# Kernel optimization log

Measured on AMD Instinct MI355X. Metric: run time of the kernel, lower is better.

The kernel has to match this reference:

```python
import jax, jax.numpy as jnp
import numpy as np

N = 20000
E = 320000
F_IN = 256
HID = 32
HEADS = 8
EDGE_DIM = HID // 4  # 8
NEG_SLOPE = 0.2


def _gat_conv(x, src, dst, e_emb, W, att_s, att_d, W_e, att_e, bias, H, C):
    """PyG-style GATConv with edge_dim, add_self_loops=True (fill_value='mean'), concat heads."""
    n = x.shape[0]
    loop = jnp.arange(n, dtype=src.dtype)
    # self-loop edge_attr = scatter-mean of edge_attr by dst (0 for isolated nodes)
    deg = jax.ops.segment_sum(jnp.ones_like(dst, dtype=x.dtype), dst, num_segments=n)
    e_mean = jax.ops.segment_sum(e_emb, dst, num_segments=n) / jnp.maximum(deg, 1.0)[:, None]
    src_a = jnp.concatenate([src, loop])
    dst_a = jnp.concatenate([dst, loop])
    e_all = jnp.concatenate([e_emb, e_mean], axis=0)  # [E+N, edge_dim]

    h = (x @ W).reshape(n, H, C)                      # [N,H,C]
    a_src = jnp.einsum('nhc,hc->nh', h, att_s)        # [N,H]
    a_dst = jnp.einsum('nhc,hc->nh', h, att_d)
    he = (e_all @ W_e).reshape(-1, H, C)              # [E+N,H,C]
    a_edge = jnp.einsum('ehc,hc->eh', he, att_e)      # [E+N,H]

    alpha = jax.nn.leaky_relu(a_src[src_a] + a_dst[dst_a] + a_edge, NEG_SLOPE)
    # segment softmax over destination nodes
    amax = jax.ops.segment_max(alpha, dst_a, num_segments=n)
    alpha = jnp.exp(alpha - amax[dst_a])
    denom = jax.ops.segment_sum(alpha, dst_a, num_segments=n)
    alpha = alpha / (denom[dst_a] + 1e-16)

    msg = h[src_a] * alpha[:, :, None]                # [E+N,H,C]
    out = jax.ops.segment_sum(msg, dst_a, num_segments=n)  # [N,H,C]
    return out.reshape(n, H * C) + bias


def setup_inputs() -> dict:
    key = jax.random.key(0)
    ks = jax.random.split(key, 16)

    def glorot(k, shape):
        fan_in, fan_out = shape[0], shape[-1]
        s = np.sqrt(6.0 / (fan_in + fan_out))
        return jax.random.uniform(k, shape, jnp.float32, -s, s)

    x = jax.random.normal(ks[0], (N, F_IN), jnp.float32)
    edge_index = jax.random.randint(ks[1], (2, E), 0, N, jnp.int32)
    edge_attr = jax.random.uniform(ks[2], (E, 2), jnp.float32)

    # spatial_embed: Linear(2 -> EDGE_DIM)
    Wse = glorot(ks[3], (2, EDGE_DIM))
    bse = jnp.zeros((EDGE_DIM,), jnp.float32)
    # conv1: in=F_IN, heads=HEADS, out=HID, edge_dim=EDGE_DIM
    W1 = glorot(ks[4], (F_IN, HEADS * HID))
    as1 = glorot(ks[5], (HEADS, HID))
    ad1 = glorot(ks[6], (HEADS, HID))
    We1 = glorot(ks[7], (EDGE_DIM, HEADS * HID))
    ae1 = glorot(ks[8], (HEADS, HID))
    b1 = jnp.zeros((HEADS * HID,), jnp.float32)
    # conv2: in=HEADS*HID, heads=1, out=HID
    W2 = glorot(ks[9], (HEADS * HID, HID))
    as2 = glorot(ks[10], (1, HID))
    ad2 = glorot(ks[11], (1, HID))
    We2 = glorot(ks[12], (EDGE_DIM, HID))
    ae2 = glorot(ks[13], (1, HID))
    b2 = jnp.zeros((HID,), jnp.float32)

    return {"x": x, "edge_index": edge_index, "edge_attr": edge_attr,
            "Wse": Wse, "bse": bse,
            "W1": W1, "as1": as1, "ad1": ad1, "We1": We1, "ae1": ae1, "b1": b1,
            "W2": W2, "as2": as2, "ad2": ad2, "We2": We2, "ae2": ae2, "b2": b2}


def reference(x, edge_index, edge_attr, Wse, bse,
              W1, as1, ad1, We1, ae1, b1,
              W2, as2, ad2, We2, ae2, b2):
    src, dst = edge_index[0], edge_index[1]
    e = jax.nn.relu(edge_attr @ Wse + bse)            # [E, EDGE_DIM]
    h = _gat_conv(x, src, dst, e, W1, as1, ad1, We1, ae1, b1, HEADS, HID)
    h = jax.nn.relu(h)                                # dropout inactive (eval)
    out = _gat_conv(h, src, dst, e, W2, as2, ad2, We2, ae2, b2, 1, HID)
    return out
```

## Files before the change

### kernel.cpp

```cpp
#include <hip/hip_runtime.h>
#include <hip/hip_bf16.h>
#include <hip/hip_fp16.h>
#include <float.h>


typedef short v8s __attribute__((ext_vector_type(8)));
typedef float v4f __attribute__((ext_vector_type(4)));

__device__ __forceinline__ ushort f2bf(float f) {
  unsigned u = __float_as_uint(f);
  u = (u + 0x7FFF + ((u >> 16) & 1)) >> 16;
  return (ushort)u;
}
__device__ __forceinline__ float bf2f(ushort h) {
  return __uint_as_float(((unsigned)h) << 16);
}
__device__ __forceinline__ unsigned pk2bf(float lo, float hi) {
  return (unsigned)f2bf(lo) | ((unsigned)f2bf(hi) << 16);
}
__device__ __forceinline__ unsigned pk2h(float lo, float hi) {
  return (unsigned)__half_as_ushort(__float2half(lo)) |
         ((unsigned)__half_as_ushort(__float2half(hi)) << 16);
}

__global__ __launch_bounds__(256) void k_pre(const int* __restrict__ dst,
                                             const float* __restrict__ W1,
                                             const float* __restrict__ We1,
                                             const float* __restrict__ ae1,
                                             const float* __restrict__ We2,
                                             const float* __restrict__ ae2,
                                             int* __restrict__ deg,
                                             ushort* __restrict__ Bt,
                                             float* __restrict__ M1,
                                             float* __restrict__ m2,
                                             int E, int DB) {
  int b = blockIdx.x;
  if (b < DB) {
    int e = b * 256 + threadIdx.x;
    if (e < E) atomicAdd(&deg[dst[e]], 1);
    return;
  }
  if (b == DB + 64) {
    int t = threadIdx.x;
    if (t < 64) {
      int k = t >> 3, h = t & 7;
      float s = 0.f;
      for (int c = 0; c < 32; c++) s += We1[k * 256 + h * 32 + c] * ae1[h * 32 + c];
      M1[k * 8 + h] = s;
    } else if (t < 72) {
      int k = t - 64;
      float s = 0.f;
      for (int c = 0; c < 32; c++) s += We2[k * 32 + c] * ae2[c];
      m2[k] = s;
    }
    return;
  }
  int b2 = b - DB;
  __shared__ float tile[32][33];
  int bx = b2 & 7, by = b2 >> 3;
  int tx = threadIdx.x & 31, ty = threadIdx.x >> 5;
  for (int r = ty; r < 32; r += 8)
    tile[r][tx] = W1[(size_t)(by * 32 + r) * 256 + bx * 32 + tx];
  __syncthreads();
  for (int r = ty; r < 32; r += 8)
    Bt[(size_t)(bx * 32 + r) * 256 + by * 32 + tx] = f2bf(tile[tx][r]);
}

__global__ __launch_bounds__(1024) void k_scan(const int* __restrict__ deg,
                                               int* __restrict__ row_ptr,
                                               int* __restrict__ cursor, int N) {
  __shared__ int part[1024];
  int tid = threadIdx.x;
  int chunk = (N + 1023) / 1024;
  int lo = tid * chunk;
  if (lo > N) lo = N;
  int hi = lo + chunk;
  if (hi > N) hi = N;
  int s = 0;
  for (int i = lo; i < hi; i++) { s += deg[i]; cursor[i] = 0; }
  part[tid] = s;
  __syncthreads();
  for (int off = 1; off < 1024; off <<= 1) {
    int v = 0;
    if (tid >= off) v = part[tid - off];
    __syncthreads();
    part[tid] += v;
    __syncthreads();
  }
  int base = part[tid] - s;
  for (int i = lo; i < hi; i++) { row_ptr[i] = base; base += deg[i]; }
  if (tid == 1023) row_ptr[N] = part[1023];
}

__global__ void k_scatter(const int* __restrict__ src, const int* __restrict__ dst,
                          const float* __restrict__ ea,
                          const float* __restrict__ Wse, const float* __restrict__ bse,
                          const float* __restrict__ M1, const float* __restrict__ m2,
                          const int* __restrict__ row_ptr, int* __restrict__ cursor,
                          char* __restrict__ rec, int E) {
  __shared__ float sW[16], sb[8], sM[64], sm2[8];
  int t = threadIdx.x;
  if (t < 16) sW[t] = Wse[t];
  if (t < 8) sb[t] = bse[t];
  if (t < 64) sM[t] = M1[t];
  if (t >= 64 && t < 72) sm2[t - 64] = m2[t - 64];
  __syncthreads();
  int i = blockIdx.x * blockDim.x + t;
  if (i >= E) return;
  float2 av = ((const float2*)ea)[i];
  float e8[8];
#pragma unroll
  for (int k = 0; k < 8; k++)
    e8[k] = fmaxf(av.x * sW[k] + av.y * sW[8 + k] + sb[k], 0.f);
  float o[8];
#pragma unroll
  for (int h = 0; h < 8; h++) {
    float s = 0.f;
#pragma unroll
    for (int k = 0; k < 8; k++) s += e8[k] * sM[k * 8 + h];
    o[h] = s;
  }
  float s2 = 0.f;
#pragma unroll
  for (int k = 0; k < 8; k++) s2 += e8[k] * sm2[k];
  int d = dst[i];
  int pos = row_ptr[d] + atomicAdd(&cursor[d], 1);
  uint4 w0, w1;
  w0.x = (unsigned)src[i];
  w0.y = pk2h(o[0], o[1]);
  w0.z = pk2h(o[2], o[3]);
  w0.w = pk2h(o[4], o[5]);
  w1.x = pk2h(o[6], o[7]);
  w1.y = __float_as_uint(s2);
  w1.z = 0; w1.w = 0;
  *(uint4*)(rec + (size_t)pos * 32)      = w0;
  *(uint4*)(rec + (size_t)pos * 32 + 16) = w1;
}

__global__ __launch_bounds__(256) void k_gemm1_mfma(const float* __restrict__ A,
                                                    const ushort* __restrict__ Bt,
                                                    const float* __restrict__ as1,
                                                    const float* __restrict__ ad1,
                                                    ushort* __restrict__ h1b,
                                                    float* __restrict__ asv,
                                                    float* __restrict__ adv, int M) {
  __shared__ ushort sA[64 * 40];
  __shared__ ushort sB[256 * 40];
  __shared__ float sas[256], sad[256];
  int t = threadIdx.x;
  int wave = t >> 6, lane = t & 63;
  int m0 = blockIdx.x * 64;
  int c = lane & 15, kg = lane >> 4;
  sas[t] = as1[t];
  sad[t] = ad1[t];
  v4f acc[4][4];
#pragma unroll
  for (int a = 0; a < 4; a++)
#pragma unroll
    for (int b = 0; b < 4; b++) acc[a][b] = (v4f)(0.f);
  int arow = t >> 2;
  int akoff = (t & 3) * 8;
  bool aval = (m0 + arow) < M;
  const float* aptr = A + (size_t)(m0 + arow) * 256 + akoff;
  const ushort* bptr = Bt + (size_t)t * 256;
  for (int k0 = 0; k0 < 256; k0 += 32) {
    float4 v0 = make_float4(0.f, 0.f, 0.f, 0.f), v1 = v0;
    if (aval) { v0 = *(const float4*)(aptr + k0); v1 = *(const float4*)(aptr + k0 + 4); }
    unsigned* dst32 = (unsigned*)&sA[arow * 40 + akoff];
    dst32[0] = pk2bf(v0.x, v0.y);
    dst32[1] = pk2bf(v0.z, v0.w);
    dst32[2] = pk2bf(v1.x, v1.y);
    dst32[3] = pk2bf(v1.z, v1.w);
    *(v8s*)&sB[t * 40 + 0]  = *(const v8s*)(bptr + k0 + 0);
    *(v8s*)&sB[t * 40 + 8]  = *(const v8s*)(bptr + k0 + 8);
    *(v8s*)&sB[t * 40 + 16] = *(const v8s*)(bptr + k0 + 16);
    *(v8s*)&sB[t * 40 + 24] = *(const v8s*)(bptr + k0 + 24);
    __syncthreads();
    v8s af[4], bfr[4];
#pragma unroll
    for (int mt = 0; mt < 4; mt++) af[mt] = *(v8s*)&sA[(mt * 16 + c) * 40 + kg * 8];
#pragma unroll
    for (int nt = 0; nt < 4; nt++) bfr[nt] = *(v8s*)&sB[(wave * 64 + nt * 16 + c) * 40 + kg * 8];
#pragma unroll
    for (int mt = 0; mt < 4; mt++)
#pragma unroll
      for (int nt = 0; nt < 4; nt++)
        acc[mt][nt] = __builtin_amdgcn_mfma_f32_16x16x32_bf16(af[mt], bfr[nt], acc[mt][nt], 0, 0, 0);
    __syncthreads();
  }
  int colbase = wave * 64;
#pragma unroll
  for (int mt = 0; mt < 4; mt++) {
#pragma unroll
    for (int i = 0; i < 4; i++) {
      int m = m0 + mt * 16 + kg * 4 + i;
      if (m < M) {
#pragma unroll
        for (int nt = 0; nt < 4; nt++)
          h1b[(size_t)m * 256 + colbase + nt * 16 + c] = f2bf(acc[mt][nt][i]);
      }
      float s1a = acc[mt][0][i] * sas[colbase + c]      + acc[mt][1][i] * sas[colbase + 16 + c];
      float s2a = acc[mt][0][i] * sad[colbase + c]      + acc[mt][1][i] * sad[colbase + 16 + c];
      float s1b = acc[mt][2][i] * sas[colbase + 32 + c] + acc[mt][3][i] * sas[colbase + 48 + c];
      float s2b = acc[mt][2][i] * sad[colbase + 32 + c] + acc[mt][3][i] * sad[colbase + 48 + c];
#pragma unroll
      for (int o = 1; o < 16; o <<= 1) {
        s1a += __shfl_xor(s1a, o);
        s2a += __shfl_xor(s2a, o);
        s1b += __shfl_xor(s1b, o);
        s2b += __shfl_xor(s2b, o);
      }
      if (c == 0 && m < M) {
        asv[(size_t)m * 8 + 2 * wave]     = s1a;
        adv[(size_t)m * 8 + 2 * wave]     = s2a;
        asv[(size_t)m * 8 + 2 * wave + 1] = s1b;
        adv[(size_t)m * 8 + 2 * wave + 1] = s2b;
      }
    }
  }
}

__global__ __launch_bounds__(64) void k_conv1(
    const int* __restrict__ row_ptr, const char* __restrict__ rec,
    const float* __restrict__ asv, const float* __restrict__ adv,
    const ushort* __restrict__ h1b, const float* __restrict__ b1,
    ushort* __restrict__ h2b, int N) {
  int n = blockIdx.x;
  int lane = threadIdx.x;
  int h = lane >> 3;
  int sub = lane & 7;
  int hh = lane & 7;
  __shared__ float sw[64 * 8];
  __shared__ int ssrc[64];
  __shared__ float sm[8], sl[8], sadv[8], smean[8];
  int begin = row_ptr[n], end = row_ptr[n + 1];
  int degr = end - begin;
  if (lane < 8) { sm[lane] = -FLT_MAX; sl[lane] = 0.f; sadv[lane] = adv[(size_t)n * 8 + lane]; }
  float aedsum = 0.f;
  float4 acc = make_float4(0.f, 0.f, 0.f, 0.f);
  for (int cs = begin; cs < end; cs += 64) {
    int c = min(64, end - cs);
    __syncthreads();
    if (lane < c) ssrc[lane] = *(const int*)(rec + (size_t)(cs + lane) * 32);
    __syncthreads();
    for (int idx = lane; idx < c * 8; idx += 64) {
      int el = idx >> 3;
      float ae = __half2float(*(const __half*)(rec + (size_t)(cs + el) * 32 + 4 + hh * 2));
      aedsum += ae;
      float a = asv[(size_t)ssrc[el] * 8 + hh] + sadv[hh] + ae;
      a = a > 0.f ? a : 0.2f * a;
      sw[idx] = a;
    }
    __syncthreads();
    float mloc = -FLT_MAX;
    for (int el = sub; el < c; el += 8) mloc = fmaxf(mloc, sw[el * 8 + h]);
#pragma unroll
    for (int o = 1; o < 8; o <<= 1) mloc = fmaxf(mloc, __shfl_xor(mloc, o));
    float mold = sm[h];
    float mnew = fmaxf(mold, mloc);
    float scale = __expf(mold - mnew);
    float lloc = 0.f;
    for (int el = sub; el < c; el += 8) {
      float w = __expf(sw[el * 8 + h] - mnew);
      sw[el * 8 + h] = w;
      lloc += w;
    }
#pragma unroll
    for (int o = 1; o < 8; o <<= 1) lloc += __shfl_xor(lloc, o);
    __syncthreads();
    if (sub == 0) { sm[h] = mnew; sl[h] = sl[h] * scale + lloc; }
    acc.x *= scale; acc.y *= scale; acc.z *= scale; acc.w *= scale;
#pragma unroll 2
    for (int el = 0; el < c; el++) {
      float w = sw[el * 8 + h];
      ushort4 hv = *(const ushort4*)(h1b + (size_t)ssrc[el] * 256 + lane * 4);
      acc.x += w * bf2f(hv.x);
      acc.y += w * bf2f(hv.y);
      acc.z += w * bf2f(hv.z);
      acc.w += w * bf2f(hv.w);
    }
  }
  aedsum += __shfl_xor(aedsum, 8);
  aedsum += __shfl_xor(aedsum, 16);
  aedsum += __shfl_xor(aedsum, 32);
  float invd = 1.f / (float)(degr > 1 ? degr : 1);
  if (lane < 8) smean[lane] = aedsum * invd;
  __syncthreads();
  float a_self = asv[(size_t)n * 8 + h] + sadv[h] + smean[h];
  a_self = a_self > 0.f ? a_self : 0.2f * a_self;
  float mold = sm[h];
  float mnew = fmaxf(mold, a_self);
  float scale = __expf(mold - mnew);
  float w_self = __expf(a_self - mnew);
  float l_fin = sl[h] * scale + w_self;
  ushort4 hs = *(const ushort4*)(h1b + (size_t)n * 256 + lane * 4);
  acc.x = acc.x * scale + w_self * bf2f(hs.x);
  acc.y = acc.y * scale + w_self * bf2f(hs.y);
  acc.z = acc.z * scale + w_self * bf2f(hs.z);
  acc.w = acc.w * scale + w_self * bf2f(hs.w);
  float inv = 1.f / (l_fin + 1e-16f);
  float4 bv = *(const float4*)(b1 + lane * 4);
  ushort4 o4;
  o4.x = f2bf(fmaxf(acc.x * inv + bv.x, 0.f));
  o4.y = f2bf(fmaxf(acc.y * inv + bv.y, 0.f));
  o4.z = f2bf(fmaxf(acc.z * inv + bv.z, 0.f));
  o4.w = f2bf(fmaxf(acc.w * inv + bv.w, 0.f));
  *(ushort4*)(h2b + (size_t)n * 256 + lane * 4) = o4;
}

__global__ __launch_bounds__(256) void k_gemm2(const ushort* __restrict__ h2b,
                                               const float* __restrict__ W2,
                                               const float* __restrict__ as2,
                                               const float* __restrict__ ad2,
                                               float* __restrict__ g2,
                                               float* __restrict__ asv2,
                                               float* __restrict__ adv2, int N) {
  __shared__ float xs[8 * 256];
  __shared__ float sas[32], sad[32];
  int t = threadIdx.x;
  if (t < 32) { sas[t] = as2[t]; sad[t] = ad2[t]; }
  int n0 = blockIdx.x * 8;
  for (int idx = t; idx < 8 * 256; idx += 256) {
    int node = n0 + (idx >> 8);
    xs[idx] = (node < N) ? bf2f(h2b[(size_t)node * 256 + (idx & 255)]) : 0.f;
  }
  __syncthreads();
  int j = t >> 5, cc = t & 31;
  int node = n0 + j;
  float acc = 0.f;
#pragma unroll 8
  for (int k = 0; k < 256; k++) acc += xs[j * 256 + k] * W2[k * 32 + cc];
  float s1 = acc * sas[cc], s2 = acc * sad[cc];
#pragma unroll
  for (int o = 1; o < 32; o <<= 1) {
    s1 += __shfl_xor(s1, o);
    s2 += __shfl_xor(s2, o);
  }
  if (node < N) {
    g2[(size_t)node * 32 + cc] = acc;
    if (cc == 0) { asv2[node] = s1; adv2[node] = s2; }
  }
}

__global__ __launch_bounds__(64) void k_conv2(
    const int* __restrict__ row_ptr, const char* __restrict__ rec,
    const float* __restrict__ asv2, const float* __restrict__ adv2,
    const float* __restrict__ g2, const float* __restrict__ b2,
    float* __restrict__ out, int N) {
  int n = blockIdx.x;
  int lane = threadIdx.x;
  int sub = lane >> 3, q = lane & 7;
  __shared__ float sw[64];
  __shared__ int ssrc[64];
  int begin = row_ptr[n], end = row_ptr[n + 1];
  int degr = end - begin;
  float advn = adv2[n];
  float m = -FLT_MAX, l = 0.f, aedsum = 0.f;
  float4 acc = make_float4(0.f, 0.f, 0.f, 0.f);
  for (int cs = begin; cs < end; cs += 64) {
    int c = min(64, end - cs);
    __syncthreads();
    float a = -FLT_MAX;
    if (lane < c) {
      const char* rp = rec + (size_t)(cs + lane) * 32;
      int s = *(const int*)rp;
      ssrc[lane] = s;
      float ae = *(const float*)(rp + 20);
      aedsum += ae;
      a = asv2[s] + advn + ae;
      a = a > 0.f ? a : 0.2f * a;
    }
    float cm = a;
#pragma unroll
    for (int o = 1; o < 64; o <<= 1) cm = fmaxf(cm, __shfl_xor(cm, o));
    float nm = fmaxf(m, cm);
    float sc = __expf(m - nm);
    float w = (lane < c) ? __expf(a - nm) : 0.f;
    float cl = w;
#pragma unroll
    for (int o = 1; o < 64; o <<= 1) cl += __shfl_xor(cl, o);
    l = l * sc + cl;
    m = nm;
    sw[lane] = w;
    __syncthreads();
    acc.x *= sc; acc.y *= sc; acc.z *= sc; acc.w *= sc;
    for (int el = sub; el < c; el += 8) {
      float w2 = sw[el];
      const float4 gv = *(const float4*)(g2 + (size_t)ssrc[el] * 32 + q * 4);
      acc.x += w2 * gv.x; acc.y += w2 * gv.y; acc.z += w2 * gv.z; acc.w += w2 * gv.w;
    }
  }
#pragma unroll
  for (int o = 1; o < 64; o <<= 1) aedsum += __shfl_xor(aedsum, o);
  float invd = 1.f / (float)(degr > 1 ? degr : 1);
  float a_self = asv2[n] + advn + aedsum * invd;
  a_self = a_self > 0.f ? a_self : 0.2f * a_self;
  float nm = fmaxf(m, a_self);
  float sc = __expf(m - nm);
  float w_self = __expf(a_self - nm);
  l = l * sc + w_self;
  acc.x *= sc; acc.y *= sc; acc.z *= sc; acc.w *= sc;
  if (sub == 0) {
    const float4 gv = *(const float4*)(g2 + (size_t)n * 32 + q * 4);
    acc.x += w_self * gv.x; acc.y += w_self * gv.y;
    acc.z += w_self * gv.z; acc.w += w_self * gv.w;
  }
#pragma unroll
  for (int o = 8; o < 64; o <<= 1) {
    acc.x += __shfl_xor(acc.x, o);
    acc.y += __shfl_xor(acc.y, o);
    acc.z += __shfl_xor(acc.z, o);
    acc.w += __shfl_xor(acc.w, o);
  }
  if (lane < 8) {
    float inv = 1.f / (l + 1e-16f);
    float4 bv = *(const float4*)(b2 + lane * 4);
    float4 o4;
    o4.x = acc.x * inv + bv.x;
    o4.y = acc.y * inv + bv.y;
    o4.z = acc.z * inv + bv.z;
    o4.w = acc.w * inv + bv.w;
    *(float4*)(out + (size_t)n * 32 + lane * 4) = o4;
  }
}

extern "C" void kernel_launch(void* const* d_in, const int* in_sizes, int n_in,
                              void* d_out, int out_size, void* d_ws, size_t ws_size,
                              hipStream_t stream) {
  (void)n_in; (void)out_size; (void)ws_size;
  const float* x   = (const float*)d_in[0];
  const int*   ei  = (const int*)d_in[1];
  const float* ea  = (const float*)d_in[2];
  const float* Wse = (const float*)d_in[3];
  const float* bse = (const float*)d_in[4];
  const float* W1  = (const float*)d_in[5];
  const float* as1 = (const float*)d_in[6];
  const float* ad1 = (const float*)d_in[7];
  const float* We1 = (const float*)d_in[8];
  const float* ae1 = (const float*)d_in[9];
  const float* b1  = (const float*)d_in[10];
  const float* W2  = (const float*)d_in[11];
  const float* as2 = (const float*)d_in[12];
  const float* ad2 = (const float*)d_in[13];
  const float* We2 = (const float*)d_in[14];
  const float* ae2 = (const float*)d_in[15];
  const float* b2  = (const float*)d_in[16];
  const int N = in_sizes[0] / 256;
  const int E = in_sizes[1] / 2;
  const int* src = ei;
  const int* dst = ei + E;

  char* base = (char*)d_ws;
  size_t off = 0;
  auto alloc = [&](size_t bytes) -> char* {
    off = (off + 255) & ~(size_t)255;
    char* p = base + off;
    off += bytes;
    return p;
  };
  int*   deg      = (int*)alloc((size_t)N * 4);
  int*   cursor   = (int*)alloc((size_t)N * 4);
  int* row_ptr    = (int*)alloc((size_t)(N + 1) * 4);
  char* rec       = alloc((size_t)E * 32);
  ushort* W1T     = (ushort*)alloc((size_t)256 * 256 * 2);
  ushort* h1b     = (ushort*)alloc((size_t)N * 256 * 2);
  float* asv1     = (float*)alloc((size_t)N * 8 * 4);
  float* adv1     = (float*)alloc((size_t)N * 8 * 4);
  ushort* h2b     = (ushort*)alloc((size_t)N * 256 * 2);
  float* g2       = (float*)alloc((size_t)N * 32 * 4);
  float* asv2     = (float*)alloc((size_t)N * 4);
  float* adv2     = (float*)alloc((size_t)N * 4);
  float* M1       = (float*)alloc(64 * 4);
  float* m2       = (float*)alloc(8 * 4);

  const int DB = (E + 255) / 256;
  hipMemsetAsync(deg, 0, (size_t)N * 4, stream);
  k_pre<<<DB + 65, 256, 0, stream>>>(dst, W1, We1, ae1, We2, ae2, deg, W1T, M1, m2, E, DB);
  k_scan<<<1, 1024, 0, stream>>>(deg, row_ptr, cursor, N);
  k_scatter<<<DB, 256, 0, stream>>>(src, dst, ea, Wse, bse, M1, m2, row_ptr, cursor,
                                    rec, E);
  k_gemm1_mfma<<<(N + 63) / 64, 256, 0, stream>>>(x, W1T, as1, ad1, h1b, asv1, adv1, N);
  k_conv1<<<N, 64, 0, stream>>>(row_ptr, rec, asv1, adv1, h1b, b1, h2b, N);
  k_gemm2<<<(N + 7) / 8, 256, 0, stream>>>(h2b, W2, as2, ad2, g2, asv2, adv2, N);
  k_conv2<<<N, 64, 0, stream>>>(row_ptr, rec, asv2, adv2, g2, b2, (float*)d_out, N);
}
```

Before: 256.2 us.

## Merge edge scatter with GEMM1 launch and fuse GEMM2 into conv1 epilogue

The edge-record scatter and the layer-1 MFMA GEMM now run as two roles of one combined launch selected by block index, so the independent work overlaps and one launch is removed. The layer-2 projection (256->32 matmul plus attention dot products) moves into the conv1 epilogue: each node's hidden vector stays in shared memory and is multiplied by a pre-blocked copy of W2 built in k_pre. This drops the bf16 h2b round trip through global memory and the separate gemm2 kernel. The cost is that every conv1 block re-reads all of W2 (32 KB, likely cache-resident) with one 64-lane block per node, and the mega kernel's shared-memory footprint is sized for the GEMM role.

```diff
diff --git a/kernel.cpp b/kernel.cpp
--- a/kernel.cpp
+++ b/kernel.cpp
@@ -29,10 +29,12 @@
                                              const float* __restrict__ ae1,
                                              const float* __restrict__ We2,
                                              const float* __restrict__ ae2,
+                                             const float* __restrict__ W2,
                                              int* __restrict__ deg,
                                              ushort* __restrict__ Bt,
                                              float* __restrict__ M1,
                                              float* __restrict__ m2,
+                                             float* __restrict__ W2B,
                                              int E, int DB) {
   int b = blockIdx.x;
   if (b < DB) {
@@ -42,6 +44,10 @@
   }
   if (b == DB + 64) {
     int t = threadIdx.x;
+    for (int i = t; i < 8192; i += 256) {
+      int k = i >> 5, cc = i & 31;
+      W2B[(size_t)(k >> 2) * 128 + cc * 4 + (k & 3)] = W2[(size_t)k * 32 + cc];
+    }
     if (t < 64) {
       int k = t >> 3, h = t & 7;
       float s = 0.f;
@@ -92,62 +98,63 @@
   if (tid == 1023) row_ptr[N] = part[1023];
 }
 
-__global__ void k_scatter(const int* __restrict__ src, const int* __restrict__ dst,
-                          const float* __restrict__ ea,
-                          const float* __restrict__ Wse, const float* __restrict__ bse,
-                          const float* __restrict__ M1, const float* __restrict__ m2,
-                          const int* __restrict__ row_ptr, int* __restrict__ cursor,
-                          char* __restrict__ rec, int E) {
-  __shared__ float sW[16], sb[8], sM[64], sm2[8];
+__global__ __launch_bounds__(256) void k_mega1(
+    const float* __restrict__ A, const ushort* __restrict__ Bt,
+    const float* __restrict__ as1, const float* __restrict__ ad1,
+    ushort* __restrict__ h1b, float* __restrict__ asv, float* __restrict__ adv, int M,
+    const int* __restrict__ src, const int* __restrict__ dst,
+    const float* __restrict__ ea, const float* __restrict__ Wse,
+    const float* __restrict__ bse, const float* __restrict__ M1,
+    const float* __restrict__ m2, const int* __restrict__ row_ptr,
+    int* __restrict__ cursor, char* __restrict__ rec, int E, int GB) {
+  __shared__ __align__(16) char smem[27648];
   int t = threadIdx.x;
-  if (t < 16) sW[t] = Wse[t];
-  if (t < 8) sb[t] = bse[t];
-  if (t < 64) sM[t] = M1[t];
-  if (t >= 64 && t < 72) sm2[t - 64] = m2[t - 64];
-  __syncthreads();
-  int i = blockIdx.x * blockDim.x + t;
-  if (i >= E) return;
-  float2 av = ((const float2*)ea)[i];
-  float e8[8];
-#pragma unroll
-  for (int k = 0; k < 8; k++)
-    e8[k] = fmaxf(av.x * sW[k] + av.y * sW[8 + k] + sb[k], 0.f);
-  float o[8];
-#pragma unroll
-  for (int h = 0; h < 8; h++) {
-    float s = 0.f;
-#pragma unroll
-    for (int k = 0; k < 8; k++) s += e8[k] * sM[k * 8 + h];
-    o[h] = s;
-  }
-  float s2 = 0.f;
-#pragma unroll
-  for (int k = 0; k < 8; k++) s2 += e8[k] * sm2[k];
-  int d = dst[i];
-  int pos = row_ptr[d] + atomicAdd(&cursor[d], 1);
-  uint4 w0, w1;
-  w0.x = (unsigned)src[i];
-  w0.y = pk2h(o[0], o[1]);
-  w0.z = pk2h(o[2], o[3]);
-  w0.w = pk2h(o[4], o[5]);
-  w1.x = pk2h(o[6], o[7]);
-  w1.y = __float_as_uint(s2);
-  w1.z = 0; w1.w = 0;
-  *(uint4*)(rec + (size_t)pos * 32)      = w0;
-  *(uint4*)(rec + (size_t)pos * 32 + 16) = w1;
-}
-
-__global__ __launch_bounds__(256) void k_gemm1_mfma(const float* __restrict__ A,
-                                                    const ushort* __restrict__ Bt,
-                                                    const float* __restrict__ as1,
-                                                    const float* __restrict__ ad1,
-                                                    ushort* __restrict__ h1b,
-                                                    float* __restrict__ asv,
-                                                    float* __restrict__ adv, int M) {
-  __shared__ ushort sA[64 * 40];
-  __shared__ ushort sB[256 * 40];
-  __shared__ float sas[256], sad[256];
-  int t = threadIdx.x;
+  if (blockIdx.x >= GB) {
+    float* sW  = (float*)smem;
+    float* sbv = sW + 16;
+    float* sM  = sbv + 8;
+    float* sm2 = sM + 64;
+    if (t < 16) sW[t] = Wse[t];
+    if (t < 8) sbv[t] = bse[t];
+    if (t < 64) sM[t] = M1[t];
+    if (t >= 64 && t < 72) sm2[t - 64] = m2[t - 64];
+    __syncthreads();
+    int i = (blockIdx.x - GB) * 256 + t;
+    if (i >= E) return;
+    float2 av = ((const float2*)ea)[i];
+    float e8[8];
+#pragma unroll
+    for (int k = 0; k < 8; k++)
+      e8[k] = fmaxf(av.x * sW[k] + av.y * sW[8 + k] + sbv[k], 0.f);
+    float o[8];
+#pragma unroll
+    for (int h = 0; h < 8; h++) {
+      float s = 0.f;
+#pragma unroll
+      for (int k = 0; k < 8; k++) s += e8[k] * sM[k * 8 + h];
+      o[h] = s;
+    }
+    float s2 = 0.f;
+#pragma unroll
+    for (int k = 0; k < 8; k++) s2 += e8[k] * sm2[k];
+    int d = dst[i];
+    int pos = row_ptr[d] + atomicAdd(&cursor[d], 1);
+    uint4 w0, w1;
+    w0.x = (unsigned)src[i];
+    w0.y = pk2h(o[0], o[1]);
+    w0.z = pk2h(o[2], o[3]);
+    w0.w = pk2h(o[4], o[5]);
+    w1.x = pk2h(o[6], o[7]);
+    w1.y = __float_as_uint(s2);
+    w1.z = 0; w1.w = 0;
+    *(uint4*)(rec + (size_t)pos * 32)      = w0;
+    *(uint4*)(rec + (size_t)pos * 32 + 16) = w1;
+    return;
+  }
+  ushort* sA = (ushort*)smem;
+  ushort* sB = (ushort*)(smem + 5120);
+  float* sas = (float*)(smem + 25600);
+  float* sad = (float*)(smem + 26624);
   int wave = t >> 6, lane = t & 63;
   int m0 = blockIdx.x * 64;
   int c = lane & 15, kg = lane >> 4;
@@ -224,7 +231,9 @@
     const int* __restrict__ row_ptr, const char* __restrict__ rec,
     const float* __restrict__ asv, const float* __restrict__ adv,
     const ushort* __restrict__ h1b, const float* __restrict__ b1,
-    ushort* __restrict__ h2b, int N) {
+    const float* __restrict__ W2B, const float* __restrict__ as2,
+    const float* __restrict__ ad2, float* __restrict__ g2,
+    float* __restrict__ asv2, float* __restrict__ adv2, int N) {
   int n = blockIdx.x;
   int lane = threadIdx.x;
   int h = lane >> 3;
@@ -233,6 +242,7 @@
   __shared__ float sw[64 * 8];
   __shared__ int ssrc[64];
   __shared__ float sm[8], sl[8], sadv[8], smean[8];
+  __shared__ float sh2[256];
   int begin = row_ptr[n], end = row_ptr[n + 1];
   int degr = end - begin;
   if (lane < 8) { sm[lane] = -FLT_MAX; sl[lane] = 0.f; sadv[lane] = adv[(size_t)n * 8 + lane]; }
@@ -300,46 +310,33 @@
   acc.w = acc.w * scale + w_self * bf2f(hs.w);
   float inv = 1.f / (l_fin + 1e-16f);
   float4 bv = *(const float4*)(b1 + lane * 4);
-  ushort4 o4;
-  o4.x = f2bf(fmaxf(acc.x * inv + bv.x, 0.f));
-  o4.y = f2bf(fmaxf(acc.y * inv + bv.y, 0.f));
-  o4.z = f2bf(fmaxf(acc.z * inv + bv.z, 0.f));
-  o4.w = f2bf(fmaxf(acc.w * inv + bv.w, 0.f));
-  *(ushort4*)(h2b + (size_t)n * 256 + lane * 4) = o4;
-}
-
-__global__ __launch_bounds__(256) void k_gemm2(const ushort* __restrict__ h2b,
-                                               const float* __restrict__ W2,
-                                               const float* __restrict__ as2,
-                                               const float* __restrict__ ad2,
-                                               float* __restrict__ g2,
-                                               float* __restrict__ asv2,
-                                               float* __restrict__ adv2, int N) {
-  __shared__ float xs[8 * 256];
-  __shared__ float sas[32], sad[32];
-  int t = threadIdx.x;
-  if (t < 32) { sas[t] = as2[t]; sad[t] = ad2[t]; }
-  int n0 = blockIdx.x * 8;
-  for (int idx = t; idx < 8 * 256; idx += 256) {
-    int node = n0 + (idx >> 8);
-    xs[idx] = (node < N) ? bf2f(h2b[(size_t)node * 256 + (idx & 255)]) : 0.f;
-  }
+  float4 h2v;
+  h2v.x = fmaxf(acc.x * inv + bv.x, 0.f);
+  h2v.y = fmaxf(acc.y * inv + bv.y, 0.f);
+  h2v.z = fmaxf(acc.z * inv + bv.z, 0.f);
+  h2v.w = fmaxf(acc.w * inv + bv.w, 0.f);
+  *(float4*)&sh2[lane * 4] = h2v;
   __syncthreads();
-  int j = t >> 5, cc = t & 31;
-  int node = n0 + j;
-  float acc = 0.f;
+  int half = lane >> 5, cc = lane & 31;
+  const float* wp = W2B + (size_t)half * 32 * 128 + cc * 4;
+  const float* hp2 = sh2 + half * 128;
+  float part = 0.f;
 #pragma unroll 8
-  for (int k = 0; k < 256; k++) acc += xs[j * 256 + k] * W2[k * 32 + cc];
-  float s1 = acc * sas[cc], s2 = acc * sad[cc];
+  for (int g = 0; g < 32; g++) {
+    float4 wv = *(const float4*)(wp + g * 128);
+    float4 hv = *(const float4*)(hp2 + g * 4);
+    part += wv.x * hv.x + wv.y * hv.y + wv.z * hv.z + wv.w * hv.w;
+  }
+  part += __shfl_xor(part, 32);
+  float s1 = part * as2[cc];
+  float s2 = part * ad2[cc];
 #pragma unroll
   for (int o = 1; o < 32; o <<= 1) {
     s1 += __shfl_xor(s1, o);
     s2 += __shfl_xor(s2, o);
   }
-  if (node < N) {
-    g2[(size_t)node * 32 + cc] = acc;
-    if (cc == 0) { asv2[node] = s1; adv2[node] = s2; }
-  }
+  if (lane < 32) g2[(size_t)n * 32 + cc] = part;
+  if (lane == 0) { asv2[n] = s1; adv2[n] = s2; }
 }
 
 __global__ __launch_bounds__(64) void k_conv2(
@@ -463,10 +460,10 @@
   int* row_ptr    = (int*)alloc((size_t)(N + 1) * 4);
   char* rec       = alloc((size_t)E * 32);
   ushort* W1T     = (ushort*)alloc((size_t)256 * 256 * 2);
+  float* W2B      = (float*)alloc((size_t)256 * 32 * 4);
   ushort* h1b     = (ushort*)alloc((size_t)N * 256 * 2);
   float* asv1     = (float*)alloc((size_t)N * 8 * 4);
   float* adv1     = (float*)alloc((size_t)N * 8 * 4);
-  ushort* h2b     = (ushort*)alloc((size_t)N * 256 * 2);
   float* g2       = (float*)alloc((size_t)N * 32 * 4);
   float* asv2     = (float*)alloc((size_t)N * 4);
   float* adv2     = (float*)alloc((size_t)N * 4);
@@ -474,13 +471,15 @@
   float* m2       = (float*)alloc(8 * 4);
 
   const int DB = (E + 255) / 256;
+  const int GB = (N + 63) / 64;
   hipMemsetAsync(deg, 0, (size_t)N * 4, stream);
-  k_pre<<<DB + 65, 256, 0, stream>>>(dst, W1, We1, ae1, We2, ae2, deg, W1T, M1, m2, E, DB);
+  k_pre<<<DB + 65, 256, 0, stream>>>(dst, W1, We1, ae1, We2, ae2, W2,
+                                     deg, W1T, M1, m2, W2B, E, DB);
   k_scan<<<1, 1024, 0, stream>>>(deg, row_ptr, cursor, N);
-  k_scatter<<<DB, 256, 0, stream>>>(src, dst, ea, Wse, bse, M1, m2, row_ptr, cursor,
-                                    rec, E);
-  k_gemm1_mfma<<<(N + 63) / 64, 256, 0, stream>>>(x, W1T, as1, ad1, h1b, asv1, adv1, N);
-  k_conv1<<<N, 64, 0, stream>>>(row_ptr, rec, asv1, adv1, h1b, b1, h2b, N);
-  k_gemm2<<<(N + 7) / 8, 256, 0, stream>>>(h2b, W2, as2, ad2, g2, asv2, adv2, N);
+  k_mega1<<<GB + DB, 256, 0, stream>>>(x, W1T, as1, ad1, h1b, asv1, adv1, N,
+                                       src, dst, ea, Wse, bse, M1, m2, row_ptr,
+                                       cursor, rec, E, GB);
+  k_conv1<<<N, 64, 0, stream>>>(row_ptr, rec, asv1, adv1, h1b, b1,
+                                W2B, as2, ad2, g2, asv2, adv2, N);
   k_conv2<<<N, 64, 0, stream>>>(row_ptr, rec, asv2, adv2, g2, b2, (float*)d_out, N);
 }
```

New measurement: 227.8 us. 11.1% less time.
